# Performance work log

Hardware: AMD Instinct MI355X
Metric: run time of the kernel (lower is better)

The kernel has to match this reference:

```python
import jax, jax.numpy as jnp
import numpy as np

SHIFT, REDUCE = 0, 1
B, T, E, H = 128, 256, 300, 256


def _make_transitions(T, B):
    # Valid left-branching sequence: S, S, (R, S)*, ending with R -> 2T-1 steps.
    t = np.zeros(2 * T - 1, dtype=np.int32)
    t[2::2] = REDUCE
    return np.tile(t[:, None], (1, B))


def setup_inputs() -> dict:
    key = jax.random.key(0)
    ks = jax.random.split(key, 8)
    stdv = 1.0 / np.sqrt(H)
    u = lambda k, shape: jax.random.uniform(k, shape, jnp.float32, -stdv, stdv)
    return {
        "x": jax.random.normal(ks[0], (B, T, E), jnp.float32),
        "transitions": jnp.asarray(_make_transitions(T, B)),
        "Wp": u(ks[1], (E, H)),
        "bp": u(ks[2], (H,)),
        "Wg": u(ks[3], (E, H)),
        "bg": u(ks[4], (H,)),
        "Wr": u(ks[5], (2 * H, 5 * H)),
        "br": u(ks[6], (5 * H,)),
    }


def reference(x, transitions, Wp, bp, Wg, bg, Wr, br):
    Bb, Tt, _ = x.shape
    Hh = Wp.shape[1]
    # buffers: c = proj_x(x); h = sigmoid(proj_x_gate(x)) * tanh(c)
    c_buf = x @ Wp + bp                      # [B, T, H]
    h_buf = jax.nn.sigmoid(x @ Wg + bg) * jnp.tanh(c_buf)
    bidx = jnp.arange(Bb)

    stack_h0 = jnp.zeros((Bb, Tt, Hh), x.dtype)
    stack_c0 = jnp.zeros((Bb, Tt, Hh), x.dtype)
    sp0 = jnp.zeros((Bb,), jnp.int32)        # stack pointer
    bp0 = jnp.full((Bb,), Tt, jnp.int32)     # buffer pointer (pop from end)

    def step(carry, trans):
        sh, sc, sp, bptr = carry
        is_shift = trans == SHIFT            # [B] bool
        # SHIFT: pop last remaining buffer entry
        nbp = jnp.where(is_shift, bptr - 1, bptr)
        src = jnp.maximum(nbp, 0)
        sft_h = h_buf[bidx, src]
        sft_c = c_buf[bidx, src]
        # REDUCE: children = top two stack entries (r = top, l = below)
        ir = jnp.maximum(sp - 1, 0)
        il = jnp.maximum(sp - 2, 0)
        hl, cl = sh[bidx, il], sc[bidx, il]
        hr, cr = sh[bidx, ir], sc[bidx, ir]
        proj = jnp.concatenate([hl, hr], axis=-1) @ Wr + br   # [B, 5H]
        i, fl, fr, g, o = jnp.split(proj, 5, axis=-1)
        c_red = (jax.nn.sigmoid(fl) * cl + jax.nn.sigmoid(fr) * cr
                 + jax.nn.sigmoid(i) * jnp.tanh(g))
        h_red = jax.nn.sigmoid(o) * jnp.tanh(c_red)
        m = is_shift[:, None]
        h_new = jnp.where(m, sft_h, h_red)
        c_new = jnp.where(m, sft_c, c_red)
        pos = jnp.where(is_shift, sp, il)    # push location
        sh = sh.at[bidx, pos].set(h_new)
        sc = sc.at[bidx, pos].set(c_new)
        sp = jnp.where(is_shift, sp + 1, sp - 1)
        return (sh, sc, sp, nbp), None

    (sh, sc, sp, _), _ = jax.lax.scan(step, (stack_h0, stack_c0, sp0, bp0), transitions)
    # root h state = top of stack, h half only
    return sh[bidx, jnp.maximum(sp - 1, 0)]
```

## Files before the change

kernel.cpp:

```cpp
#include <hip/hip_runtime.h>
#include <hip/hip_fp16.h>
#include <math.h>

#define B_ 128
#define T_ 256
#define E_ 300
#define H_ 256
#define N5_ 1280
#define NSTEPS 511
#define DMAX 8

typedef _Float16 half8_t __attribute__((ext_vector_type(8)));
typedef float float4_t __attribute__((ext_vector_type(4)));
typedef int i4v __attribute__((ext_vector_type(4)));
typedef unsigned int u4v __attribute__((ext_vector_type(4)));

__device__ __forceinline__ float sigm_p(float x){ return 1.f/(1.f + expf(-x)); }
__device__ __forceinline__ float sigm(float x){ return __builtin_amdgcn_rcpf(1.f + __expf(-x)); }
__device__ __forceinline__ float ftanh(float x){
  float xc = fminf(15.f, fmaxf(-15.f, x));
  float e = __expf(-2.f*xc);
  return (1.f - e) * __builtin_amdgcn_rcpf(1.f + e);
}

__global__ __launch_bounds__(64) void k0a_scale(const float* __restrict__ Wr,
    float* __restrict__ scales){
  const int n = blockIdx.x, t = threadIdx.x;
  float m = 0.f;
  #pragma unroll
  for (int j=0;j<4;j++) m = fmaxf(m, fabsf(Wr[(size_t)(t+64*j)*N5_ + n]));
  #pragma unroll
  for (int off=32; off; off>>=1) m = fmaxf(m, __shfl_xor(m, off, 64));
  if (t==0) scales[n] = fmaxf(m, 1e-20f) * (1.f/127.f);
}

__global__ __launch_bounds__(256) void k0b_quant(const float* __restrict__ Wr,
    const float* __restrict__ scales, uint4* __restrict__ W4){
  int idx = blockIdx.x*256 + threadIdx.x;
  if (idx >= 20480) return;
  const int f    = idx >> 6;
  const int lane = idx & 63;
  const int w    = f / 80;
  const int r80  = f - w*80;
  const int g    = r80 >> 4;
  const int cg   = (r80 >> 2) & 3;
  const int kc   = r80 & 3;
  const int ml   = lane & 15, quad = lane >> 4;
  const int col  = g*256 + w*64 + cg*16 + ml;
  const float inv = 1.f / scales[col];
  unsigned int d[4];
  #pragma unroll
  for (int r=0; r<4; r++){
    unsigned int acc = 0;
    #pragma unroll
    for (int j=0; j<4; j++){
      const int k = kc*64 + quad*16 + r*4 + j;
      float wv = Wr[(size_t)k*N5_ + col];
      int q = (int)rintf(wv * inv);
      q = q > 127 ? 127 : (q < -127 ? -127 : q);
      acc |= ((unsigned int)(q & 255)) << (8*j);
    }
    d[r] = acc;
  }
  uint4 v; v.x=d[0]; v.y=d[1]; v.z=d[2]; v.w=d[3];
  W4[idx] = v;
}

__global__ __launch_bounds__(256) void k1_proj(
    const float* __restrict__ x, const float* __restrict__ Wp, const float* __restrict__ bp,
    const float* __restrict__ Wg, const float* __restrict__ bg,
    _Float16* __restrict__ h2, _Float16* __restrict__ c2){
  __shared__ __align__(16) _Float16 As [64*32];
  __shared__ __align__(16) _Float16 BsP[64*32];
  __shared__ __align__(16) _Float16 BsG[64*32];
  const int tid = threadIdx.x;
  const int row0 = blockIdx.x * 64;
  const int n0   = blockIdx.y * 64;
  const int wave = tid >> 6, lane = tid & 63;
  const int ml = lane & 15, quad = lane >> 4;
  float4_t accP[4], accG[4];
  #pragma unroll
  for (int i=0;i<4;i++){ accP[i]=(float4_t)(0.f); accG[i]=(float4_t)(0.f); }
  const int ar = tid >> 2, ak = (tid & 3) * 8;
  const int bk = tid >> 3, bn = (tid & 7) * 8;
  for (int kk = 0; kk < E_; kk += 32){
    __syncthreads();
    {
      const float* src = x + (size_t)(row0 + ar)*E_ + kk + ak;
      float v[8];
      #pragma unroll
      for (int q=0;q<2;q++){
        if (kk + ak + q*4 + 4 <= E_){
          float4_t f = *(const float4_t*)(src + q*4);
          v[q*4+0]=f.x; v[q*4+1]=f.y; v[q*4+2]=f.z; v[q*4+3]=f.w;
        } else {
          #pragma unroll
          for (int j=0;j<4;j++){ int kg = kk+ak+q*4+j; v[q*4+j] = (kg<E_) ? src[q*4+j] : 0.f; }
        }
      }
      #pragma unroll
      for (int j=0;j<8;j++) As[ar*32 + ak + j] = (_Float16)v[j];
    }
    {
      const int kg = kk + bk;
      if (kg < E_){
        const float* sp_ = Wp + (size_t)kg*H_ + n0 + bn;
        const float* sg_ = Wg + (size_t)kg*H_ + n0 + bn;
        float4_t p0 = *(const float4_t*)sp_, p1 = *(const float4_t*)(sp_+4);
        float4_t g0 = *(const float4_t*)sg_, g1 = *(const float4_t*)(sg_+4);
        float pv[8]={p0.x,p0.y,p0.z,p0.w,p1.x,p1.y,p1.z,p1.w};
        float gv[8]={g0.x,g0.y,g0.z,g0.w,g1.x,g1.y,g1.z,g1.w};
        #pragma unroll
        for (int j=0;j<8;j++){ BsP[(bn+j)*32+bk]=(_Float16)pv[j]; BsG[(bn+j)*32+bk]=(_Float16)gv[j]; }
      } else {
        #pragma unroll
        for (int j=0;j<8;j++){ BsP[(bn+j)*32+bk]=(_Float16)0.f; BsG[(bn+j)*32+bk]=(_Float16)0.f; }
      }
    }
    __syncthreads();
    half8_t a = *(const half8_t*)&As[(wave*16 + ml)*32 + quad*8];
    #pragma unroll
    for (int nt=0; nt<4; nt++){
      half8_t b1 = *(const half8_t*)&BsP[(nt*16 + ml)*32 + quad*8];
      accP[nt] = __builtin_amdgcn_mfma_f32_16x16x32_f16(a, b1, accP[nt], 0,0,0);
      half8_t b2 = *(const half8_t*)&BsG[(nt*16 + ml)*32 + quad*8];
      accG[nt] = __builtin_amdgcn_mfma_f32_16x16x32_f16(a, b2, accG[nt], 0,0,0);
    }
  }
  #pragma unroll
  for (int nt=0; nt<4; nt++){
    #pragma unroll
    for (int r=0;r<4;r++){
      int row = row0 + wave*16 + quad*4 + r;
      int col = n0 + nt*16 + ml;
      float c = accP[nt][r] + bp[col];
      float g = accG[nt][r] + bg[col];
      float h = sigm_p(g) * tanhf(c);
      size_t o = (size_t)row*H_ + col;
      c2[o] = (_Float16)c;
      h2[o] = (_Float16)h;
    }
  }
}

__global__ __launch_bounds__(256) void k2_rproj(
    const _Float16* __restrict__ h2, const float* __restrict__ Wr, const float* __restrict__ br,
    _Float16* __restrict__ R2){
  __shared__ __align__(16) _Float16 As[64*32];
  __shared__ __align__(16) _Float16 Bs[64*32];
  const int tid = threadIdx.x;
  const int row0 = blockIdx.x*64, n0 = blockIdx.y*64;
  const int wave = tid>>6, lane = tid&63, ml = lane&15, quad = lane>>4;
  float4_t acc[4];
  #pragma unroll
  for (int i=0;i<4;i++) acc[i]=(float4_t)(0.f);
  const int ar = tid>>2, ak = (tid&3)*8;
  const int bk = tid>>3, bn = (tid&7)*8;
  for (int kk=0; kk<H_; kk+=32){
    __syncthreads();
    *(half8_t*)&As[ar*32+ak] = *(const half8_t*)(h2 + (size_t)(row0+ar)*H_ + kk + ak);
    {
      const float* src = Wr + (size_t)(256 + kk + bk)*N5_ + n0 + bn;
      float4_t f0 = *(const float4_t*)src, f1 = *(const float4_t*)(src+4);
      float v[8]={f0.x,f0.y,f0.z,f0.w,f1.x,f1.y,f1.z,f1.w};
      #pragma unroll
      for (int j=0;j<8;j++) Bs[(bn+j)*32+bk] = (_Float16)v[j];
    }
    __syncthreads();
    half8_t a = *(const half8_t*)&As[(wave*16+ml)*32 + quad*8];
    #pragma unroll
    for (int nt=0; nt<4; nt++){
      half8_t b8 = *(const half8_t*)&Bs[(nt*16+ml)*32 + quad*8];
      acc[nt] = __builtin_amdgcn_mfma_f32_16x16x32_f16(a, b8, acc[nt], 0,0,0);
    }
  }
  #pragma unroll
  for (int nt=0; nt<4; nt++){
    #pragma unroll
    for (int r=0;r<4;r++){
      int row = row0 + wave*16 + quad*4 + r;
      int col = n0 + nt*16 + ml;
      R2[(size_t)row*N5_ + col] = (_Float16)(acc[nt][r] + br[col]);
    }
  }
}

#define K3_LDS_BYTES 86016

#define DECL8(g) u4v bf##g##_0_0, bf##g##_0_1, bf##g##_0_2, bf##g##_0_3, \
                     bf##g##_1_0, bf##g##_1_1, bf##g##_1_2, bf##g##_1_3;
#define LOAD8(g) \
  bf##g##_0_0 = wb[((g)*16 + 0)*64]; bf##g##_0_1 = wb[((g)*16 + 1)*64]; \
  bf##g##_0_2 = wb[((g)*16 + 2)*64]; bf##g##_0_3 = wb[((g)*16 + 3)*64]; \
  bf##g##_1_0 = wb[((g)*16 + 4)*64]; bf##g##_1_1 = wb[((g)*16 + 5)*64]; \
  bf##g##_1_2 = wb[((g)*16 + 6)*64]; bf##g##_1_3 = wb[((g)*16 + 7)*64];

#define MFA(ACC, AF, BF) asm("v_mfma_i32_16x16x64_i8 %0, %1, %2, %0" \
    : "+v"(ACC) : "v"(AF), "a"(BF));
#define MFV(ACC, AF, BF) asm("v_mfma_i32_16x16x64_i8 %0, %1, %2, %0" \
    : "+v"(ACC) : "v"(AF), "v"(BF));
#define FENCE_IN2(A0,A1)  asm volatile("s_nop 1" : "+v"(A0), "+v"(A1));
#define FENCE_OUT2(A0,A1) asm volatile("s_nop 7\n\ts_nop 7" : "+v"(A0), "+v"(A1));
#define BARRIER() asm volatile("s_waitcnt lgkmcnt(0)\n\ts_barrier" ::: "memory")

#define GCHAIN2(g, DST) { \
  i4v A0={0,0,0,0}, A1={0,0,0,0}; \
  FENCE_IN2(A0,A1) \
  MFA(A0,af0,bf##g##_0_0) MFA(A1,af0,bf##g##_1_0) \
  MFA(A0,af1,bf##g##_0_1) MFA(A1,af1,bf##g##_1_1) \
  MFA(A0,af2,bf##g##_0_2) MFA(A1,af2,bf##g##_1_2) \
  MFA(A0,af3,bf##g##_0_3) MFA(A1,af3,bf##g##_1_3) \
  FENCE_OUT2(A0,A1) \
  DST = hsel ? A1.x : A0.x; }

#define GCHAIN2_G4(DST) { \
  const u4v og00=lwg4[0],   og01=lwg4[64],  og02=lwg4[128], og03=lwg4[192]; \
  const u4v og10=lwg4[256], og11=lwg4[320], og12=lwg4[384], og13=lwg4[448]; \
  i4v A0={0,0,0,0}, A1={0,0,0,0}; \
  FENCE_IN2(A0,A1) \
  MFV(A0,af0,og00) MFV(A1,af0,og10) \
  MFV(A0,af1,og01) MFV(A1,af1,og11) \
  MFV(A0,af2,og02) MFV(A1,af2,og12) \
  MFV(A0,af3,og03) MFV(A1,af3,og13) \
  FENCE_OUT2(A0,A1) \
  DST = hsel ? A1.x : A0.x; }

#define PAIR_STEP(IDX, RD, WR) { \
  BARRIER(); \
  float a0=(float)pA0, a1=(float)pA1, a2=(float)pA2, a3=(float)pA3, a4=(float)pA4; \
  const float tc = (float)pAc; \
  const u4v* sRD = (const u4v*)(sI8 + (RD)*H_); \
  const u4v af0 = sRD[quad], af1 = sRD[4+quad], af2 = sRD[8+quad], af3 = sRD[12+quad]; \
  { int rrow = 253-(IDX); if (rrow < 0) rrow = 0; \
    const _Float16* rr = R2 + ((size_t)b*T_ + rrow)*N5_ + col; \
    pA0=rr[0]; pA1=rr[256]; pA2=rr[512]; pA3=rr[768]; pA4=rr[1024]; \
    int crow = 252-(IDX); if (crow < 0) crow = 0; \
    pAc = c2[((size_t)b*T_ + crow)*H_ + col]; } \
  int d0,d1,d2,d3,d4; \
  GCHAIN2_G4(d4)  a4 += scf4*(float)d4; \
  GCHAIN2(0, d0)  a0 += scf0*(float)d0; \
  GCHAIN2(1, d1)  a1 += scf1*(float)d1; \
  GCHAIN2(2, d2)  a2 += scf2*(float)d2; \
  GCHAIN2(3, d3)  a3 += scf3*(float)d3; \
  const float cnew = sigm(a1)*cl + sigm(a2)*cr + sigm(a0)*ftanh(a3); \
  const float hnew = sigm(a4)*ftanh(cnew); \
  sI8[(WR)*H_ + col] = (char)(int)rintf(hnew*127.f); \
  cl = cnew; cr = tc; \
}

__global__ __launch_bounds__(512, 2) void k3_scan(
    const int* __restrict__ trans, const _Float16* __restrict__ h2, const _Float16* __restrict__ c2,
    const _Float16* __restrict__ R2, const uint4* __restrict__ W4,
    const float* __restrict__ scales, const float* __restrict__ Wr,
    const float* __restrict__ br, float* __restrict__ out){
  extern __shared__ char smem[];
  u4v*   wlds  = (u4v*)smem;
  float* sh_   = (float*)(smem + 65536);
  float* sc_   = (float*)(smem + 73728);
  char*  sI8   = (char*)(smem + 81920);
  const u4v* sI4 = (const u4v*)(smem + 81920);
  int* trs     = (int*)(smem + 83968);

  const int b = blockIdx.x, tid = threadIdx.x;
  const int lane = tid & 63, w8 = tid >> 6;
  const int quad = (lane >> 4) & 3;
  const int hsel = (lane >> 4) & 1;
  const int col  = (w8 << 5) + (lane & 31);
  const int w4   = w8 >> 1, cg0 = (w8 & 1) * 2;

  const u4v* WB4v = (const u4v*)W4;
  const u4v* wb   = WB4v + ((size_t)w4*80 + cg0*4)*64 + lane;

  DECL8(0) DECL8(1) DECL8(2) DECL8(3)
  LOAD8(0) LOAD8(1) LOAD8(2) LOAD8(3)

  #pragma unroll
  for (int t=0; t<8; t++){
    const int flat = t*512 + tid;
    const int fd   = flat >> 6;
    const int dl   = flat & 63;
    const int w8d  = fd >> 3;
    const int ii   = (fd >> 2) & 1;
    const int kc   = fd & 3;
    const int cg   = (w8d & 1)*2 + ii;
    const int srcf = (w8d >> 1)*80 + 4*16 + cg*4 + kc;
    wlds[flat] = WB4v[(size_t)srcf*64 + dl];
  }
  const u4v* lwg4 = wlds + (size_t)w8*512 + lane;

  const float scf0 = scales[col       ] * (1.f/127.f);
  const float scf1 = scales[col +  256] * (1.f/127.f);
  const float scf2 = scales[col +  512] * (1.f/127.f);
  const float scf3 = scales[col +  768] * (1.f/127.f);
  const float scf4 = scales[col + 1024] * (1.f/127.f);

  trs[tid] = (tid < NSTEPS) ? trans[(size_t)tid*B_ + b] : 1;
  for (int i = tid; i < DMAX*H_; i += 512){ sh_[i]=0.f; sc_[i]=0.f; sI8[i]=0; }

  int myok = 1;
  if (tid < NSTEPS){ int e = (tid>=2 && (tid&1)==0) ? 1 : 0; if (trs[tid]!=e) myok=0; }
  const int ok = __syncthreads_and(myok);

  if (ok){
    const size_t hb = (size_t)b*T_*H_;
    const _Float16 h255 = h2[hb + 255*H_ + col];
    float cl = (float)c2[hb + 255*H_ + col];
    float cr = (float)c2[hb + 254*H_ + col];
    _Float16 pA0,pA1,pA2,pA3,pA4,pAc;
    { const _Float16* rr = R2 + ((size_t)b*T_ + 254)*N5_ + col;
      pA0=rr[0]; pA1=rr[256]; pA2=rr[512]; pA3=rr[768]; pA4=rr[1024];
      pAc = c2[hb + 253*H_ + col]; }
    sI8[col] = (char)(int)rintf((float)h255 * 127.f);
    #pragma unroll 1
    for (int i=0; i<254; i+=2){
      PAIR_STEP(i,   0, 1)
      PAIR_STEP(i+1, 1, 0)
    }
    {
      BARRIER();
      float a0=(float)pA0, a1=(float)pA1, a2=(float)pA2, a3=(float)pA3, a4=(float)pA4;
      const u4v* sRD = (const u4v*)sI8;
      const u4v af0 = sRD[quad], af1 = sRD[4+quad], af2 = sRD[8+quad], af3 = sRD[12+quad];
      int d0,d1,d2,d3,d4;
      GCHAIN2_G4(d4)  a4 += scf4*(float)d4;
      GCHAIN2(0, d0)  a0 += scf0*(float)d0;
      GCHAIN2(1, d1)  a1 += scf1*(float)d1;
      GCHAIN2(2, d2)  a2 += scf2*(float)d2;
      GCHAIN2(3, d3)  a3 += scf3*(float)d3;
      const float cnew = sigm(a1)*cl + sigm(a2)*cr + sigm(a0)*ftanh(a3);
      const float hnew = sigm(a4)*ftanh(cnew);
      if (lane < 32) out[(size_t)b*H_ + col] = hnew;
    }
    return;
  }

  int sp = 0, bptr = T_, prev_src = -1;
  for (int step=0; step<NSTEPS; step++){
    __syncthreads();
    const int tr = trs[step];
    if (tr == 0){
      const int nbp = bptr - 1;
      const int src = nbp > 0 ? nbp : 0;
      const int slot = sp < 0 ? 0 : (sp > DMAX-1 ? DMAX-1 : sp);
      const size_t o = ((size_t)b*T_ + src)*H_ + col;
      const float wh = (float)h2[o], wc = (float)c2[o];
      sh_[slot*H_+col] = wh;
      sc_[slot*H_+col] = wc;
      sI8[slot*H_+col] = (char)(int)rintf(wh * 127.f);
      sp += 1; bptr = nbp; prev_src = src;
    } else {
      int ir = sp-1 > 0 ? sp-1 : 0;
      int il = sp-2 > 0 ? sp-2 : 0;
      ir = ir > DMAX-1 ? DMAX-1 : ir;
      il = il > DMAX-1 ? DMAX-1 : il;
      const int tg = prev_src;
      const float cl = sc_[il*H_+col];
      const float cr = sc_[ir*H_+col];
      const u4v af0 = sI4[il*16 +  0 + quad];
      const u4v af1 = sI4[il*16 +  4 + quad];
      const u4v af2 = sI4[il*16 +  8 + quad];
      const u4v af3 = sI4[il*16 + 12 + quad];
      float a0,a1,a2,a3,a4;
      if (tg >= 0){
        const _Float16* rr = R2 + ((size_t)b*T_ + tg)*N5_ + col;
        a0=(float)rr[0]; a1=(float)rr[256]; a2=(float)rr[512]; a3=(float)rr[768]; a4=(float)rr[1024];
      } else {
        a0=br[col]; a1=br[col+256]; a2=br[col+512]; a3=br[col+768]; a4=br[col+1024];
      }
      int d0,d1,d2,d3,d4;
      GCHAIN2_G4(d4)  a4 += scf4*(float)d4;
      GCHAIN2(0, d0)  a0 += scf0*(float)d0;
      GCHAIN2(1, d1)  a1 += scf1*(float)d1;
      GCHAIN2(2, d2)  a2 += scf2*(float)d2;
      GCHAIN2(3, d3)  a3 += scf3*(float)d3;
      if (tg < 0){
        for (int k=0; k<H_; k++){
          const float hrk = sh_[ir*H_+k];
          const float* wr = Wr + (size_t)(256+k)*N5_ + col;
          a0 += hrk*wr[0]; a1 += hrk*wr[256]; a2 += hrk*wr[512];
          a3 += hrk*wr[768]; a4 += hrk*wr[1024];
        }
      }
      const float cnew = sigm(a1)*cl + sigm(a2)*cr + sigm(a0)*ftanh(a3);
      const float hnew = sigm(a4)*ftanh(cnew);
      const int wq = (int)rintf(hnew * 127.f);
      __syncthreads();
      sh_[il*H_+col] = hnew;
      sc_[il*H_+col] = cnew;
      sI8[il*H_+col] = (char)wq;
      sp -= 1; prev_src = -1;
    }
  }
  __syncthreads();
  int fs = sp-1 > 0 ? sp-1 : 0;
  fs = fs > DMAX-1 ? DMAX-1 : fs;
  if (lane < 32) out[(size_t)b*H_ + col] = sh_[fs*H_+col];
}

extern "C" void kernel_launch(void* const* d_in, const int* in_sizes, int n_in,
                              void* d_out, int out_size, void* d_ws, size_t ws_size,
                              hipStream_t stream){
  const float* x    = (const float*)d_in[0];
  const int*   trn  = (const int*)  d_in[1];
  const float* Wp   = (const float*)d_in[2];
  const float* bp   = (const float*)d_in[3];
  const float* Wg   = (const float*)d_in[4];
  const float* bg   = (const float*)d_in[5];
  const float* Wr   = (const float*)d_in[6];
  const float* br   = (const float*)d_in[7];
  float* out = (float*)d_out;
  char* w = (char*)d_ws;
  _Float16* h2   = (_Float16*)(w);
  _Float16* c2   = (_Float16*)(w + (size_t)16777216);
  _Float16* R2   = (_Float16*)(w + (size_t)33554432);
  uint4*    W4   = (uint4*)   (w + (size_t)117440512);
  float*    scl  = (float*)   (w + (size_t)117768192);

  hipLaunchKernelGGL(k0a_scale, dim3(1280),    dim3(64),  0, stream, Wr, scl);
  hipLaunchKernelGGL(k0b_quant, dim3(80),      dim3(256), 0, stream, Wr, scl, W4);
  hipLaunchKernelGGL(k1_proj,   dim3(512, 4),  dim3(256), 0, stream, x, Wp, bp, Wg, bg, h2, c2);
  hipLaunchKernelGGL(k2_rproj,  dim3(512, 20), dim3(256), 0, stream, h2, Wr, br, R2);
  hipLaunchKernelGGL(k3_scan,   dim3(128),     dim3(512), K3_LDS_BYTES, stream, trn, h2, c2, R2, W4, scl, Wr, br, out);
}
```

Baseline: 517.5 us.

## Pre-transpose Wr to fp16 and use 128x128 tiles in the R-projection GEMM

Adds a kernel that converts the right half of Wr to a transposed fp16 copy. The R-projection GEMM then loads both operands with vectorized half8 loads instead of converting and scattering fp32 into LDS. That GEMM also moves from 64x64 to 128x128 block tiles with a 4x4 MFMA grid per wave for more operand reuse. Separately, the gate-4 int8 MFMA chain in the scan is moved after the other gates. The costs are one extra kernel launch, a small workspace buffer, and higher register pressure in the GEMM.

```diff
diff --git a/kernel.cpp b/kernel.cpp
--- a/kernel.cpp
+++ b/kernel.cpp
@@ -64,6 +64,13 @@
   }
   uint4 v; v.x=d[0]; v.y=d[1]; v.z=d[2]; v.w=d[3];
   W4[idx] = v;
+}
+
+__global__ __launch_bounds__(256) void k0d_wrt(const float* __restrict__ Wr,
+    _Float16* __restrict__ Wr2t){
+  int idx = blockIdx.x*256 + threadIdx.x;
+  const int col = idx >> 8, k = idx & 255;
+  Wr2t[(size_t)col*H_ + k] = (_Float16)Wr[(size_t)(256 + k)*N5_ + col];
 }
 
 __global__ __launch_bounds__(256) void k1_proj(
@@ -144,45 +151,55 @@
 }
 
 __global__ __launch_bounds__(256) void k2_rproj(
-    const _Float16* __restrict__ h2, const float* __restrict__ Wr, const float* __restrict__ br,
-    _Float16* __restrict__ R2){
-  __shared__ __align__(16) _Float16 As[64*32];
-  __shared__ __align__(16) _Float16 Bs[64*32];
+    const _Float16* __restrict__ h2, const _Float16* __restrict__ Wr2t,
+    const float* __restrict__ br, _Float16* __restrict__ R2){
+  __shared__ __align__(16) _Float16 As[128*32];
+  __shared__ __align__(16) _Float16 Bs[128*32];
   const int tid = threadIdx.x;
-  const int row0 = blockIdx.x*64, n0 = blockIdx.y*64;
+  const int row0 = blockIdx.x*128, col0 = blockIdx.y*128;
   const int wave = tid>>6, lane = tid&63, ml = lane&15, quad = lane>>4;
-  float4_t acc[4];
-  #pragma unroll
-  for (int i=0;i<4;i++) acc[i]=(float4_t)(0.f);
-  const int ar = tid>>2, ak = (tid&3)*8;
-  const int bk = tid>>3, bn = (tid&7)*8;
-  for (int kk=0; kk<H_; kk+=32){
+  const int wr = wave>>1, wc = wave&1;
+
+  float4_t acc[4][4];
+  #pragma unroll
+  for (int i=0;i<4;i++)
+    #pragma unroll
+    for (int j=0;j<4;j++) acc[i][j]=(float4_t)(0.f);
+
+  for (int ks=0; ks<8; ks++){
+    const int k0 = ks*32;
     __syncthreads();
-    *(half8_t*)&As[ar*32+ak] = *(const half8_t*)(h2 + (size_t)(row0+ar)*H_ + kk + ak);
-    {
-      const float* src = Wr + (size_t)(256 + kk + bk)*N5_ + n0 + bn;
-      float4_t f0 = *(const float4_t*)src, f1 = *(const float4_t*)(src+4);
-      float v[8]={f0.x,f0.y,f0.z,f0.w,f1.x,f1.y,f1.z,f1.w};
+    #pragma unroll
+    for (int p=0; p<2; p++){
+      const int flat = p*256 + tid;
+      const int r  = flat >> 2;
+      const int kq = (flat & 3) * 8;
+      *(half8_t*)&As[r*32 + kq] = *(const half8_t*)(h2   + (size_t)(row0 + r)*H_ + k0 + kq);
+      *(half8_t*)&Bs[r*32 + kq] = *(const half8_t*)(Wr2t + (size_t)(col0 + r)*H_ + k0 + kq);
+    }
+    __syncthreads();
+    half8_t a[4], b[4];
+    #pragma unroll
+    for (int mi=0; mi<4; mi++) a[mi] = *(const half8_t*)&As[(wr*64 + mi*16 + ml)*32 + quad*8];
+    #pragma unroll
+    for (int ni=0; ni<4; ni++) b[ni] = *(const half8_t*)&Bs[(wc*64 + ni*16 + ml)*32 + quad*8];
+    #pragma unroll
+    for (int mi=0; mi<4; mi++)
       #pragma unroll
-      for (int j=0;j<8;j++) Bs[(bn+j)*32+bk] = (_Float16)v[j];
-    }
-    __syncthreads();
-    half8_t a = *(const half8_t*)&As[(wave*16+ml)*32 + quad*8];
-    #pragma unroll
-    for (int nt=0; nt<4; nt++){
-      half8_t b8 = *(const half8_t*)&Bs[(nt*16+ml)*32 + quad*8];
-      acc[nt] = __builtin_amdgcn_mfma_f32_16x16x32_f16(a, b8, acc[nt], 0,0,0);
-    }
-  }
-  #pragma unroll
-  for (int nt=0; nt<4; nt++){
-    #pragma unroll
-    for (int r=0;r<4;r++){
-      int row = row0 + wave*16 + quad*4 + r;
-      int col = n0 + nt*16 + ml;
-      R2[(size_t)row*N5_ + col] = (_Float16)(acc[nt][r] + br[col]);
-    }
-  }
+      for (int ni=0; ni<4; ni++)
+        acc[mi][ni] = __builtin_amdgcn_mfma_f32_16x16x32_f16(a[mi], b[ni], acc[mi][ni], 0,0,0);
+  }
+
+  #pragma unroll
+  for (int mi=0; mi<4; mi++)
+    #pragma unroll
+    for (int ni=0; ni<4; ni++)
+      #pragma unroll
+      for (int r=0; r<4; r++){
+        const int row = row0 + wr*64 + mi*16 + quad*4 + r;
+        const int col = col0 + wc*64 + ni*16 + ml;
+        R2[(size_t)row*N5_ + col] = (_Float16)(acc[mi][ni][r] + br[col]);
+      }
 }
 
 #define K3_LDS_BYTES 86016
@@ -237,11 +254,11 @@
     int crow = 252-(IDX); if (crow < 0) crow = 0; \
     pAc = c2[((size_t)b*T_ + crow)*H_ + col]; } \
   int d0,d1,d2,d3,d4; \
-  GCHAIN2_G4(d4)  a4 += scf4*(float)d4; \
   GCHAIN2(0, d0)  a0 += scf0*(float)d0; \
   GCHAIN2(1, d1)  a1 += scf1*(float)d1; \
   GCHAIN2(2, d2)  a2 += scf2*(float)d2; \
   GCHAIN2(3, d3)  a3 += scf3*(float)d3; \
+  GCHAIN2_G4(d4)  a4 += scf4*(float)d4; \
   const float cnew = sigm(a1)*cl + sigm(a2)*cr + sigm(a0)*ftanh(a3); \
   const float hnew = sigm(a4)*ftanh(cnew); \
   sI8[(WR)*H_ + col] = (char)(int)rintf(hnew*127.f); \
@@ -322,11 +339,11 @@
       const u4v* sRD = (const u4v*)sI8;
       const u4v af0 = sRD[quad], af1 = sRD[4+quad], af2 = sRD[8+quad], af3 = sRD[12+quad];
       int d0,d1,d2,d3,d4;
-      GCHAIN2_G4(d4)  a4 += scf4*(float)d4;
       GCHAIN2(0, d0)  a0 += scf0*(float)d0;
       GCHAIN2(1, d1)  a1 += scf1*(float)d1;
       GCHAIN2(2, d2)  a2 += scf2*(float)d2;
       GCHAIN2(3, d3)  a3 += scf3*(float)d3;
+      GCHAIN2_G4(d4)  a4 += scf4*(float)d4;
       const float cnew = sigm(a1)*cl + sigm(a2)*cr + sigm(a0)*ftanh(a3);
       const float hnew = sigm(a4)*ftanh(cnew);
       if (lane < 32) out[(size_t)b*H_ + col] = hnew;
@@ -368,11 +385,11 @@
         a0=br[col]; a1=br[col+256]; a2=br[col+512]; a3=br[col+768]; a4=br[col+1024];
       }
       int d0,d1,d2,d3,d4;
-      GCHAIN2_G4(d4)  a4 += scf4*(float)d4;
       GCHAIN2(0, d0)  a0 += scf0*(float)d0;
       GCHAIN2(1, d1)  a1 += scf1*(float)d1;
       GCHAIN2(2, d2)  a2 += scf2*(float)d2;
       GCHAIN2(3, d3)  a3 += scf3*(float)d3;
+      GCHAIN2_G4(d4)  a4 += scf4*(float)d4;
       if (tg < 0){
         for (int k=0; k<H_; k++){
           const float hrk = sh_[ir*H_+k];
@@ -415,10 +432,12 @@
   _Float16* R2   = (_Float16*)(w + (size_t)33554432);
   uint4*    W4   = (uint4*)   (w + (size_t)117440512);
   float*    scl  = (float*)   (w + (size_t)117768192);
-
-  hipLaunchKernelGGL(k0a_scale, dim3(1280),    dim3(64),  0, stream, Wr, scl);
-  hipLaunchKernelGGL(k0b_quant, dim3(80),      dim3(256), 0, stream, Wr, scl, W4);
-  hipLaunchKernelGGL(k1_proj,   dim3(512, 4),  dim3(256), 0, stream, x, Wp, bp, Wg, bg, h2, c2);
-  hipLaunchKernelGGL(k2_rproj,  dim3(512, 20), dim3(256), 0, stream, h2, Wr, br, R2);
-  hipLaunchKernelGGL(k3_scan,   dim3(128),     dim3(512), K3_LDS_BYTES, stream, trn, h2, c2, R2, W4, scl, Wr, br, out);
-}
+  _Float16* Wr2t = (_Float16*)(w + (size_t)117773312);
+
+  hipLaunchKernelGGL(k0a_scale, dim3(1280),     dim3(64),  0, stream, Wr, scl);
+  hipLaunchKernelGGL(k0b_quant, dim3(80),       dim3(256), 0, stream, Wr, scl, W4);
+  hipLaunchKernelGGL(k0d_wrt,   dim3(1280),     dim3(256), 0, stream, Wr, Wr2t);
+  hipLaunchKernelGGL(k1_proj,   dim3(512, 4),   dim3(256), 0, stream, x, Wp, bp, Wg, bg, h2, c2);
+  hipLaunchKernelGGL(k2_rproj,  dim3(256, 10),  dim3(256), 0, stream, h2, Wr2t, br, R2);
+  hipLaunchKernelGGL(k3_scan,   dim3(128),      dim3(512), K3_LDS_BYTES, stream, trn, h2, c2, R2, W4, scl, Wr, br, out);
+}
```

Result: faster. 465.5 us (-10.1%).
